# Kernel tuning notes

Hardware: AMD Instinct MI355X
Metric: run time of the kernel (lower is better)

Reference implementation:

```python
import jax, jax.numpy as jnp
import numpy as np

NUM_HEAD = 8
HEAD_SIZE = 32  # attention_size 256 / 8 heads


def setup_inputs() -> dict:
    key = jax.random.key(0)
    ks = jax.random.split(key, 10)
    B, S, H, A = 2, 4096, 256, 256
    x = jax.random.normal(ks[0], (B, S, H), dtype=jnp.float32)
    mask = jax.random.randint(ks[1], (B, S), 0, 2) > 0  # bool key-padding mask
    s = 0.02
    wq = jax.random.normal(ks[2], (A, H), dtype=jnp.float32) * s
    bq = jax.random.normal(ks[3], (A,), dtype=jnp.float32) * s
    wk = jax.random.normal(ks[4], (A, H), dtype=jnp.float32) * s
    bk = jax.random.normal(ks[5], (A,), dtype=jnp.float32) * s
    wv = jax.random.normal(ks[6], (A, H), dtype=jnp.float32) * s
    bv = jax.random.normal(ks[7], (A,), dtype=jnp.float32) * s
    wo = jax.random.normal(ks[8], (H, A), dtype=jnp.float32) * s
    bo = jax.random.normal(ks[9], (H,), dtype=jnp.float32) * s
    return {"x": x, "mask": mask, "wq": wq, "bq": bq, "wk": wk, "bk": bk,
            "wv": wv, "bv": bv, "wo": wo, "bo": bo}


def reference(x, mask, wq, bq, wk, bk, wv, bv, wo, bo):
    B, S, _ = x.shape
    # QKV projections -> [B, S, n_head, head_size]
    q = (x @ wq.T + bq).reshape(B, S, NUM_HEAD, HEAD_SIZE)
    k = (x @ wk.T + bk).reshape(B, S, NUM_HEAD, HEAD_SIZE)
    v = (x @ wv.T + bv).reshape(B, S, NUM_HEAD, HEAD_SIZE)
    # scores [B, H, Sq, Sk]
    attn = jnp.einsum('bqhd,bkhd->bhqk', q, k) / jnp.sqrt(
        jnp.asarray(HEAD_SIZE, dtype=x.dtype))
    # attn*mask - 1e5*~mask  ==  where(mask, attn, -1e5)
    attn = jnp.where(mask[:, None, None, :], attn, jnp.asarray(-100000.0, dtype=x.dtype))
    p = jax.nn.softmax(attn, axis=-1)
    o = jnp.einsum('bhqk,bkhd->bqhd', p, v).reshape(B, S, NUM_HEAD * HEAD_SIZE)
    return o @ wo.T + bo
```

## Files before the change

kernel.cpp:

```cpp
#include <hip/hip_runtime.h>

#define DEV __device__ __forceinline__

typedef __attribute__((ext_vector_type(8)))  short bf16x8;
typedef __attribute__((ext_vector_type(4)))  short s16x4;
typedef __attribute__((ext_vector_type(16))) float f32x16;

constexpr int SB = 2;
constexpr int SS = 4096;
constexpr int SH = 256;
constexpr int NHEAD = 8, HD = 32;
constexpr int M_TOK = SB * SS;
constexpr int NQKV = 3 * SH;

constexpr size_t OFF_CNT  = 0;
constexpr size_t OFF_BIAS = 256;
constexpr size_t OFF_XB   = OFF_BIAS + 32768;
constexpr size_t OFF_WQKV = OFF_XB + (size_t)M_TOK * SH * 2;
constexpr size_t OFF_BQKV = OFF_WQKV + (size_t)NQKV * SH * 2;
constexpr size_t OFF_WOB  = OFF_BQKV + 4096;
constexpr size_t OFF_BO   = OFF_WOB + (size_t)SH * SH * 2;
constexpr size_t OFF_Q    = OFF_BO + 1024;
constexpr size_t OFF_K    = OFF_Q + (size_t)M_TOK * SH * 2;
constexpr size_t OFF_V    = OFF_K + (size_t)M_TOK * SH * 2;
constexpr size_t OFF_VT   = OFF_V + (size_t)M_TOK * SH * 2;
constexpr size_t OFF_O    = OFF_VT + (size_t)M_TOK * SH * 2;
constexpr size_t WS_NEED  = OFF_O + (size_t)M_TOK * SH * 2;

DEV short f2bf(float f) {
  unsigned u = __builtin_bit_cast(unsigned, f);
  u = (u + 0x7FFFu + ((u >> 16) & 1u)) >> 16;
  return (short)u;
}

DEV float bf2f(short s) {
  return __builtin_bit_cast(float, ((unsigned)(unsigned short)s) << 16);
}

DEV float exp2_(float x) {
#if __has_builtin(__builtin_amdgcn_exp2f)
  return __builtin_amdgcn_exp2f(x);
#else
  float r;
  asm("v_exp_f32 %0, %1\n\ts_nop 0" : "=v"(r) : "v"(x));
  return r;
#endif
}

DEV unsigned cvtpk(float lo, float hi) {
  unsigned r;
  asm("v_cvt_pk_bf16_f32 %0, %1, %2" : "=v"(r) : "v"(lo), "v"(hi));
  return r;
}

DEV void plswap(unsigned& a, unsigned& b) {
  asm("v_permlane32_swap_b32 %0, %1" : "+v"(a), "+v"(b));
}

DEV float bperm_f(int srclane, float v) {
  int r = __builtin_amdgcn_ds_bpermute(srclane * 4, __builtin_bit_cast(int, v));
  return __builtin_bit_cast(float, r);
}

DEV void gll16(const short* g, short* l) {
  __builtin_amdgcn_global_load_lds(
      (const __attribute__((address_space(1))) void*)g,
      (__attribute__((address_space(3))) void*)l, 16, 0, 0);
}

__global__ void prep_kernel(const float* __restrict__ x,
    const float* __restrict__ wq, const float* __restrict__ bq,
    const float* __restrict__ wk, const float* __restrict__ bk,
    const float* __restrict__ wv, const float* __restrict__ bv,
    const float* __restrict__ wo, const float* __restrict__ bo,
    short* __restrict__ xb, short* __restrict__ Wqkv, float* __restrict__ bqkv,
    short* __restrict__ wob, float* __restrict__ bof) {
  const float QS = (float)(1.4426950408889634 / 5.656854249492381);
  long i = ((long)blockIdx.x * 256 + threadIdx.x) * 8;
  const long NX = (long)M_TOK * SH;
  const long NW = (long)NQKV * SH;
  if (i < NX) {
    const float4* s = (const float4*)(x + i);
    float4 f0 = s[0], f1 = s[1];
    bf16x8 o;
    o[0]=f2bf(f0.x); o[1]=f2bf(f0.y); o[2]=f2bf(f0.z); o[3]=f2bf(f0.w);
    o[4]=f2bf(f1.x); o[5]=f2bf(f1.y); o[6]=f2bf(f1.z); o[7]=f2bf(f1.w);
    *(bf16x8*)(xb + i) = o;
    return;
  }
  i -= NX;
  if (i < NW) {
    int n = (int)(i >> 8), kk = (int)(i & 255);
    int tn = n >> 8, rr = n & 255;
    const float* src = (tn == 0 ? wq : (tn == 1 ? wk : wv)) + rr * 256 + kk;
    float sc = tn == 0 ? QS : 1.f;
    float4 f0 = *(const float4*)src, f1 = *(const float4*)(src + 4);
    bf16x8 o;
    o[0]=f2bf(f0.x*sc); o[1]=f2bf(f0.y*sc); o[2]=f2bf(f0.z*sc); o[3]=f2bf(f0.w*sc);
    o[4]=f2bf(f1.x*sc); o[5]=f2bf(f1.y*sc); o[6]=f2bf(f1.z*sc); o[7]=f2bf(f1.w*sc);
    *(bf16x8*)(Wqkv + i) = o;
    return;
  }
  i -= NW;
  if (i < NQKV) {
    int n = (int)i;
#pragma unroll
    for (int j = 0; j < 8; ++j) {
      int nn = n + j, tn = nn >> 8, rr = nn & 255;
      const float* src = tn == 0 ? bq : (tn == 1 ? bk : bv);
      bqkv[nn] = src[rr] * (tn == 0 ? QS : 1.f);
    }
    return;
  }
  i -= NQKV;
  if (i < (long)SH * SH) {
    const float4* s = (const float4*)(wo + i);
    float4 f0 = s[0], f1 = s[1];
    bf16x8 o;
    o[0]=f2bf(f0.x); o[1]=f2bf(f0.y); o[2]=f2bf(f0.z); o[3]=f2bf(f0.w);
    o[4]=f2bf(f1.x); o[5]=f2bf(f1.y); o[6]=f2bf(f1.z); o[7]=f2bf(f1.w);
    *(bf16x8*)(wob + i) = o;
    return;
  }
  i -= (long)SH * SH;
  if (i < SH) {
#pragma unroll
    for (int j = 0; j < 8; ++j) bof[i + j] = bo[i + j];
  }
}

template <int MODE>
__global__ __launch_bounds__(256) void gemm_kernel(
    const short* __restrict__ Ag, const short* __restrict__ Bg,
    const float* __restrict__ bias,
    short* __restrict__ q, short* __restrict__ k, short* __restrict__ v,
    float* __restrict__ outf) {
  __shared__ __align__(16) short lA[8192];
  __shared__ __align__(16) short lB[4096];
  const int tid = threadIdx.x;
  const int lane = tid & 63, w = tid >> 6;
  const int wm = w >> 1, wn = w & 1;
  const int hi = lane >> 5, l31 = lane & 31;
  const int mb = blockIdx.x, nb = blockIdx.y;
  f32x16 acc0, acc1;
#pragma unroll
  for (int i = 0; i < 16; ++i) { acc0[i] = 0.f; acc1[i] = 0.f; }
  auto stage = [&](int kb) {
#pragma unroll
    for (int i = 0; i < 4; ++i) {
      int g = w * 256 + i * 64 + lane;
      int kg = g >> 7, m = g & 127;
      gll16(Ag + (size_t)(mb * 128 + m) * 256 + kb * 64 + kg * 8, lA + (size_t)g * 8);
    }
#pragma unroll
    for (int i = 0; i < 2; ++i) {
      int g = w * 128 + i * 64 + lane;
      int kg = g >> 6, n = g & 63;
      gll16(Bg + (size_t)(nb * 64 + n) * 256 + kb * 64 + kg * 8, lB + (size_t)g * 8);
    }
  };
  stage(0);
  for (int kb = 0; kb < 4; ++kb) {
    __syncthreads();
#pragma unroll
    for (int ks = 0; ks < 4; ++ks) {
      bf16x8 af0 = *(const bf16x8*)(lA + ((2 * ks + hi) * 128 + wm * 64 + l31) * 8);
      bf16x8 af1 = *(const bf16x8*)(lA + ((2 * ks + hi) * 128 + wm * 64 + 32 + l31) * 8);
      bf16x8 bf  = *(const bf16x8*)(lB + ((2 * ks + hi) * 64 + wn * 32 + l31) * 8);
      acc0 = __builtin_amdgcn_mfma_f32_32x32x16_bf16(af0, bf, acc0, 0, 0, 0);
      acc1 = __builtin_amdgcn_mfma_f32_32x32x16_bf16(af1, bf, acc1, 0, 0, 0);
    }
    __syncthreads();
    if (kb < 3) stage(kb + 1);
  }
  const int ncol = nb * 64 + wn * 32 + l31;
  const float bval = bias[ncol];
  if (MODE == 0) {
    const int tensor = nb >> 2;
    short* dst = tensor == 0 ? q : (tensor == 1 ? k : v);
    const int a = (nb & 3) * 64 + wn * 32 + l31;
    const int hh = a >> 5, d = a & 31;
#pragma unroll
    for (int mt = 0; mt < 2; ++mt) {
      const f32x16& acc = mt == 0 ? acc0 : acc1;
#pragma unroll
      for (int r = 0; r < 16; ++r) {
        int gm = mb * 128 + wm * 64 + mt * 32 + (r & 3) + 8 * (r >> 2) + 4 * hi;
        int bb = gm >> 12, ss = gm & 4095;
        dst[(((size_t)bb * NHEAD + hh) * SS + ss) * HD + d] = f2bf(acc[r] + bval);
      }
    }
  } else {
#pragma unroll
    for (int mt = 0; mt < 2; ++mt) {
      const f32x16& acc = mt == 0 ? acc0 : acc1;
#pragma unroll
      for (int r = 0; r < 16; ++r) {
        int gm = mb * 128 + wm * 64 + mt * 32 + (r & 3) + 8 * (r >> 2) + 4 * hi;
        outf[(size_t)gm * SH + ncol] = acc[r] + bval;
      }
    }
  }
}

__global__ void scan_mask_kernel(const unsigned char* __restrict__ m,
                                 int* __restrict__ idxC, int* __restrict__ cnts) {
  __shared__ int f_mis, f_off4, f_3f;
  __shared__ int ts[256];
  const int tid = threadIdx.x, b = blockIdx.x;
  if (tid == 0) { f_mis = 0; f_off4 = 0; f_3f = 0; }
  __syncthreads();
  int lm = 0, lo4 = 0, l3f = 0;
  for (int i = tid; i < 8192; i += 256) {
    unsigned char c = m[i];
    if (c) {
      if (i & 3) lm = 1;
      if ((i & 7) == 4) lo4 = 1;
      if ((i & 3) == 3 && c == 0x3F) l3f = 1;
    }
  }
  if (lm)  atomicOr(&f_mis, 1);
  if (lo4) atomicOr(&f_off4, 1);
  if (l3f) atomicOr(&f_3f, 1);
  __syncthreads();
  const int f = !f_mis ? (f_off4 ? 1 : 3) : (f_3f ? 2 : 0);
  int bits = 0;
  const int rbase = b * 4096 + tid * 16;
#pragma unroll
  for (int j = 0; j < 16; ++j) {
    int r = rbase + j;
    bool on;
    if (f == 0)      on = m[r] != 0;
    else if (f == 1) on = m[(size_t)r * 4] != 0;
    else if (f == 2) on = m[(size_t)r * 4 + 3] != 0;
    else             on = m[(size_t)r * 8] != 0;
    bits |= (int)on << j;
  }
  const int cnt = __popc(bits);
  ts[tid] = cnt;
  __syncthreads();
  for (int off = 1; off < 256; off <<= 1) {
    int u = (tid >= off) ? ts[tid - off] : 0;
    __syncthreads();
    ts[tid] += u;
    __syncthreads();
  }
  const int total = ts[255];
  int pos = ts[tid] - cnt;
  int* idxB = idxC + b * 4096;
  if (total == 0) {
    for (int j = tid; j < 4096; j += 256) idxB[j] = j;
    if (tid == 0) { cnts[b] = 4096; cnts[2 + b] = 4096; }
    return;
  }
#pragma unroll
  for (int j = 0; j < 16; ++j)
    if ((bits >> j) & 1) { idxB[pos] = tid * 16 + j; ++pos; }
  int cntpad = (total + 255) & ~255;
  if (cntpad < 256) cntpad = 256;
  for (int j = total + tid; j < cntpad; j += 256) idxB[j] = -1;
  if (tid == 0) { cnts[b] = cntpad; cnts[2 + b] = total; }
}

__global__ __launch_bounds__(256) void gather_kv_kernel(const short* __restrict__ K,
    const short* __restrict__ V, const int* __restrict__ idxC, const int* __restrict__ cnts,
    short* __restrict__ Kc, short* __restrict__ Vt) {
  const int bh = blockIdx.y, b = bh >> 3;
  const int jb = blockIdx.x * 64;
  if (jb >= cnts[b]) return;
  __shared__ short t[64][33];
  const int tid = threadIdx.x;
  const int s = tid >> 2, g = tid & 3;
  const int ix = idxC[b * 4096 + jb + s];
  bf16x8 kvv{}, vvv{};
  if (ix >= 0) {
    kvv = *(const bf16x8*)(K + ((size_t)bh * SS + ix) * HD + g * 8);
    vvv = *(const bf16x8*)(V + ((size_t)bh * SS + ix) * HD + g * 8);
  }
  *(bf16x8*)(Kc + ((size_t)bh * SS + jb + s) * HD + g * 8) = kvv;
#pragma unroll
  for (int j = 0; j < 8; ++j) t[s][g * 8 + j] = vvv[j];
  __syncthreads();
  const int d = tid >> 3, gs = tid & 7;
  bf16x8 out;
#pragma unroll
  for (int j = 0; j < 8; ++j) out[j] = t[gs * 8 + j][d];
  *(bf16x8*)(Vt + ((size_t)bh * HD + d) * SS + jb + gs * 8) = out;
}

__global__ __launch_bounds__(256, 2) void attn_kernel(const short* __restrict__ Q,
    const short* __restrict__ Kc, const short* __restrict__ Vt,
    const int* __restrict__ cnts,
    short* __restrict__ OP0, short* __restrict__ OP1, float* __restrict__ Lp) {
  __shared__ __align__(16) short sK[4096];
  __shared__ __align__(16) short sV[4096];
  const int tid = threadIdx.x;
  const int lane = tid & 63, wave = tid >> 6;
  const int hi = lane >> 5, l31 = lane & 31;
  const int qblk = blockIdx.x, bh = blockIdx.y, half = blockIdx.z;
  const int b = bh >> 3, h = bh & 7;
  const int Lh = cnts[b] >> 1;
  const int NIT = Lh >> 7;
  const int kv0 = half * Lh;
  const short* Kb = Kc + ((size_t)bh * SS + kv0) * HD;
  const short* Vb = Vt + (size_t)bh * HD * SS + kv0;
  const int qbase = qblk * 256 + wave * 64;
  const short* QrowA = Q + ((size_t)bh * SS + qbase + l31) * HD;
  const short* QrowB = QrowA + 32 * HD;
  const bf16x8 qa0 = *(const bf16x8*)(QrowA + hi * 8);
  const bf16x8 qa1 = *(const bf16x8*)(QrowA + 16 + hi * 8);
  const bf16x8 qb0 = *(const bf16x8*)(QrowB + hi * 8);
  const bf16x8 qb1 = *(const bf16x8*)(QrowB + 16 + hi * 8);
  f32x16 zro;
#pragma unroll
  for (int i = 0; i < 16; ++i) zro[i] = 0.f;
  f32x16 accA = zro, accB = zro;
  float lsA[4] = {0.f, 0.f, 0.f, 0.f};
  float lsB[4] = {0.f, 0.f, 0.f, 0.f};
  const int kgd = tid >> 6, kkv = tid & 63;
  const int vdv = tid & 31, vgk = tid >> 5;
  const short* kvsrc = Kb + (size_t)kkv * HD + kgd * 8;
  const short* vvsrc = Vb + (size_t)vdv * SS + vgk * 8;
  short* kdst0 = sK + ((size_t)kgd * 128 + kkv) * 8;
  short* kdst1 = kdst0 + 64 * 8;
  short* vdst0 = sV + ((size_t)vgk * 32 + vdv) * 8;
  short* vdst1 = vdst0 + 8 * 32 * 8;
  bf16x8 stgK0 = *(const bf16x8*)kvsrc;
  bf16x8 stgK1 = *(const bf16x8*)(kvsrc + 64 * HD);
  bf16x8 stgV0 = *(const bf16x8*)vvsrc;
  bf16x8 stgV1 = *(const bf16x8*)(vvsrc + 64);

  auto pack = [&](const f32x16& p, bf16x8& A, bf16x8& B) {
    unsigned a0 = cvtpk(p[0], p[1]),   a1 = cvtpk(p[2], p[3]);
    unsigned b0 = cvtpk(p[4], p[5]),   b1 = cvtpk(p[6], p[7]);
    plswap(a0, b0); plswap(a1, b1);
    unsigned c0 = cvtpk(p[8], p[9]),   c1 = cvtpk(p[10], p[11]);
    unsigned d0 = cvtpk(p[12], p[13]), d1 = cvtpk(p[14], p[15]);
    plswap(c0, d0); plswap(c1, d1);
    union { unsigned u[4]; bf16x8 v; } x, y;
    x.u[0] = a0; x.u[1] = a1; x.u[2] = b0; x.u[3] = b1;
    y.u[0] = c0; y.u[1] = c1; y.u[2] = d0; y.u[3] = d1;
    A = x.v; B = y.v;
  };

  for (int kt = 0; kt < NIT; ++kt) {
    __syncthreads();
    *(bf16x8*)kdst0 = stgK0;
    *(bf16x8*)kdst1 = stgK1;
    *(bf16x8*)vdst0 = stgV0;
    *(bf16x8*)vdst1 = stgV1;
    __syncthreads();
    if (kt + 1 < NIT) {
      const short* ks = kvsrc + (size_t)(kt + 1) * 128 * HD;
      stgK0 = *(const bf16x8*)ks;
      stgK1 = *(const bf16x8*)(ks + 64 * HD);
      const short* vs = vvsrc + (kt + 1) * 128;
      stgV0 = *(const bf16x8*)vs;
      stgV1 = *(const bf16x8*)(vs + 64);
    }
#pragma unroll
    for (int sub = 0; sub < 2; ++sub) {
      const int kb = sub * 64;
      const bf16x8 a00 = *(const bf16x8*)(sK + ((hi)*128 + kb + l31) * 8);
      const bf16x8 a01 = *(const bf16x8*)(sK + ((2 + hi) * 128 + kb + l31) * 8);
      const bf16x8 a10 = *(const bf16x8*)(sK + ((hi)*128 + kb + 32 + l31) * 8);
      const bf16x8 a11 = *(const bf16x8*)(sK + ((2 + hi) * 128 + kb + 32 + l31) * 8);
      const bf16x8 vb0 = *(const bf16x8*)(sV + ((sub * 8 + hi) * 32 + l31) * 8);
      const bf16x8 vb1 = *(const bf16x8*)(sV + ((sub * 8 + 2 + hi) * 32 + l31) * 8);
      const bf16x8 vb2 = *(const bf16x8*)(sV + ((sub * 8 + 4 + hi) * 32 + l31) * 8);
      const bf16x8 vb3 = *(const bf16x8*)(sV + ((sub * 8 + 6 + hi) * 32 + l31) * 8);
      f32x16 sA0 = __builtin_amdgcn_mfma_f32_32x32x16_bf16(a00, qa0, zro, 0, 0, 0);
      sA0 = __builtin_amdgcn_mfma_f32_32x32x16_bf16(a01, qa1, sA0, 0, 0, 0);
      f32x16 sA1 = __builtin_amdgcn_mfma_f32_32x32x16_bf16(a10, qa0, zro, 0, 0, 0);
      sA1 = __builtin_amdgcn_mfma_f32_32x32x16_bf16(a11, qa1, sA1, 0, 0, 0);
      f32x16 sB0 = __builtin_amdgcn_mfma_f32_32x32x16_bf16(a00, qb0, zro, 0, 0, 0);
      sB0 = __builtin_amdgcn_mfma_f32_32x32x16_bf16(a01, qb1, sB0, 0, 0, 0);
      f32x16 sB1 = __builtin_amdgcn_mfma_f32_32x32x16_bf16(a10, qb0, zro, 0, 0, 0);
      sB1 = __builtin_amdgcn_mfma_f32_32x32x16_bf16(a11, qb1, sB1, 0, 0, 0);
      f32x16 p;
#pragma unroll
      for (int r = 0; r < 16; ++r) { p[r] = exp2_(sA0[r]); lsA[r & 3] += p[r]; }
      bf16x8 pa1, pa2;
      pack(p, pa1, pa2);
#pragma unroll
      for (int r = 0; r < 16; ++r) { p[r] = exp2_(sA1[r]); lsA[r & 3] += p[r]; }
      bf16x8 pa3, pa4;
      pack(p, pa3, pa4);
      accA = __builtin_amdgcn_mfma_f32_32x32x16_bf16(pa1, vb0, accA, 0, 0, 0);
      accA = __builtin_amdgcn_mfma_f32_32x32x16_bf16(pa2, vb1, accA, 0, 0, 0);
      accA = __builtin_amdgcn_mfma_f32_32x32x16_bf16(pa3, vb2, accA, 0, 0, 0);
      accA = __builtin_amdgcn_mfma_f32_32x32x16_bf16(pa4, vb3, accA, 0, 0, 0);
#pragma unroll
      for (int r = 0; r < 16; ++r) { p[r] = exp2_(sB0[r]); lsB[r & 3] += p[r]; }
      bf16x8 pb1, pb2;
      pack(p, pb1, pb2);
#pragma unroll
      for (int r = 0; r < 16; ++r) { p[r] = exp2_(sB1[r]); lsB[r & 3] += p[r]; }
      bf16x8 pb3, pb4;
      pack(p, pb3, pb4);
      accB = __builtin_amdgcn_mfma_f32_32x32x16_bf16(pb1, vb0, accB, 0, 0, 0);
      accB = __builtin_amdgcn_mfma_f32_32x32x16_bf16(pb2, vb1, accB, 0, 0, 0);
      accB = __builtin_amdgcn_mfma_f32_32x32x16_bf16(pb3, vb2, accB, 0, 0, 0);
      accB = __builtin_amdgcn_mfma_f32_32x32x16_bf16(pb4, vb3, accB, 0, 0, 0);
    }
  }
  float fsA = (lsA[0] + lsA[1]) + (lsA[2] + lsA[3]);
  float fsB = (lsB[0] + lsB[1]) + (lsB[2] + lsB[3]);
  fsA += __shfl_xor(fsA, 32);
  fsB += __shfl_xor(fsB, 32);
  short* OP = half ? OP1 : OP0;
#pragma unroll
  for (int r = 0; r < 16; ++r) {
    int qq = (r & 3) + 8 * (r >> 2) + 4 * hi;
    int mA = b * SS + qbase + qq;
    OP[(size_t)mA * SH + h * HD + l31] = f2bf(accA[r]);
    int mB = mA + 32;
    OP[(size_t)mB * SH + h * HD + l31] = f2bf(accB[r]);
    float lvA = bperm_f(qq, fsA);
    float lvB = bperm_f(qq, fsB);
    if (l31 == 0) {
      Lp[((size_t)half * 16 + bh) * SS + qbase + qq] = lvA;
      Lp[((size_t)half * 16 + bh) * SS + qbase + 32 + qq] = lvB;
    }
  }
}

__global__ __launch_bounds__(256) void combine_kernel(const short* __restrict__ P0,
    const short* __restrict__ P1, const float* __restrict__ Lp,
    const int* __restrict__ cnts, short* __restrict__ Ow) {
  int t = blockIdx.x * 256 + threadIdx.x;
  int m = t >> 6, c4 = (t & 63) * 4;
  int b = m >> 12, s = m & 4095, h = c4 >> 5;
  s16x4 o0 = *(const s16x4*)(P0 + (size_t)m * SH + c4);
  s16x4 o1 = *(const s16x4*)(P1 + (size_t)m * SH + c4);
  int bh = b * 8 + h;
  float npad = (float)(cnts[b] - cnts[2 + b]);
  float l = Lp[(size_t)bh * SS + s] + Lp[((size_t)16 + bh) * SS + s] - npad;
  float rcp = 1.f / l;
  s16x4 out;
#pragma unroll
  for (int j = 0; j < 4; ++j) out[j] = f2bf((bf2f(o0[j]) + bf2f(o1[j])) * rcp);
  *(s16x4*)(Ow + (size_t)m * SH + c4) = out;
}

extern "C" void kernel_launch(void* const* d_in, const int* in_sizes, int n_in,
                              void* d_out, int out_size, void* d_ws, size_t ws_size,
                              hipStream_t stream) {
  (void)in_sizes; (void)n_in; (void)out_size;
  if (ws_size < WS_NEED) return;
  const float* x  = (const float*)d_in[0];
  const unsigned char* mask = (const unsigned char*)d_in[1];
  const float* wq = (const float*)d_in[2];
  const float* bq = (const float*)d_in[3];
  const float* wk = (const float*)d_in[4];
  const float* bk = (const float*)d_in[5];
  const float* wv = (const float*)d_in[6];
  const float* bv = (const float*)d_in[7];
  const float* wo = (const float*)d_in[8];
  const float* bo = (const float*)d_in[9];
  char* ws = (char*)d_ws;
  int*   cnts    = (int*)(ws + OFF_CNT);
  short* xb      = (short*)(ws + OFF_XB);
  short* Wqkv    = (short*)(ws + OFF_WQKV);
  float* bqkv    = (float*)(ws + OFF_BQKV);
  short* wob     = (short*)(ws + OFF_WOB);
  float* bof     = (float*)(ws + OFF_BO);
  short* Qw      = (short*)(ws + OFF_Q);
  short* Kw      = (short*)(ws + OFF_K);
  short* Vw      = (short*)(ws + OFF_V);
  short* Vtw     = (short*)(ws + OFF_VT);
  short* Kc      = (short*)(ws + OFF_XB);
  int*   idxC    = (int*)(ws + OFF_WQKV);
  short* OP0     = (short*)(ws + OFF_K);
  short* OP1     = (short*)(ws + OFF_V);
  float* Lp      = (float*)(ws + OFF_O);

  prep_kernel<<<1153, 256, 0, stream>>>(x, wq, bq, wk, bk, wv, bv, wo, bo,
                                        xb, Wqkv, bqkv, wob, bof);
  gemm_kernel<0><<<dim3(64, 12), 256, 0, stream>>>(xb, Wqkv, bqkv, Qw, Kw, Vw, nullptr);
  scan_mask_kernel<<<2, 256, 0, stream>>>(mask, idxC, cnts);
  gather_kv_kernel<<<dim3(64, 16), 256, 0, stream>>>(Kw, Vw, idxC, cnts, Kc, Vtw);
  attn_kernel<<<dim3(16, 16, 2), 256, 0, stream>>>(Qw, Kc, Vtw, cnts, OP0, OP1, Lp);
  combine_kernel<<<2048, 256, 0, stream>>>(OP0, OP1, Lp, cnts, OP0);
  gemm_kernel<1><<<dim3(64, 4), 256, 0, stream>>>(OP0, wob, bof,
                                                  nullptr, nullptr, nullptr, (float*)d_out);
}
```

Measured before the change: 85.73 us.

## Stage GEMM tiles through registers and prefetch next k-block during MFMA

Replaces the direct global-to-LDS loads in the projection GEMM with ordinary vector loads into registers, followed by an explicit store to LDS. The next k-block's global loads are now issued before the MFMA loop on the current tile, so memory latency can overlap with compute instead of stalling after each block. It also changes the global access pattern so each thread reads 8 consecutive bf16 along K for a row, which should give coalesced 128-byte row segments. The cost is extra VGPRs for the staging registers and explicit LDS write instructions.

```diff
diff --git a/kernel.cpp b/kernel.cpp
--- a/kernel.cpp
+++ b/kernel.cpp
@@ -60,12 +60,6 @@
 DEV float bperm_f(int srclane, float v) {
   int r = __builtin_amdgcn_ds_bpermute(srclane * 4, __builtin_bit_cast(int, v));
   return __builtin_bit_cast(float, r);
-}
-
-DEV void gll16(const short* g, short* l) {
-  __builtin_amdgcn_global_load_lds(
-      (const __attribute__((address_space(1))) void*)g,
-      (__attribute__((address_space(3))) void*)l, 16, 0, 0);
 }
 
 __global__ void prep_kernel(const float* __restrict__ x,
@@ -145,23 +139,27 @@
   f32x16 acc0, acc1;
 #pragma unroll
   for (int i = 0; i < 16; ++i) { acc0[i] = 0.f; acc1[i] = 0.f; }
-  auto stage = [&](int kb) {
-#pragma unroll
-    for (int i = 0; i < 4; ++i) {
-      int g = w * 256 + i * 64 + lane;
-      int kg = g >> 7, m = g & 127;
-      gll16(Ag + (size_t)(mb * 128 + m) * 256 + kb * 64 + kg * 8, lA + (size_t)g * 8);
-    }
-#pragma unroll
-    for (int i = 0; i < 2; ++i) {
-      int g = w * 128 + i * 64 + lane;
-      int kg = g >> 6, n = g & 63;
-      gll16(Bg + (size_t)(nb * 64 + n) * 256 + kb * 64 + kg * 8, lB + (size_t)g * 8);
-    }
+  bf16x8 ra[4], rb[2];
+  const int am = tid >> 3, ak = tid & 7;
+  auto gload = [&](int kb) {
+#pragma unroll
+    for (int p = 0; p < 4; ++p)
+      ra[p] = *(const bf16x8*)(Ag + (size_t)(mb * 128 + p * 32 + am) * 256 + kb * 64 + ak * 8);
+#pragma unroll
+    for (int p = 0; p < 2; ++p)
+      rb[p] = *(const bf16x8*)(Bg + (size_t)(nb * 64 + p * 32 + am) * 256 + kb * 64 + ak * 8);
   };
-  stage(0);
+  gload(0);
   for (int kb = 0; kb < 4; ++kb) {
     __syncthreads();
+#pragma unroll
+    for (int p = 0; p < 4; ++p)
+      *(bf16x8*)(lA + (ak * 128 + p * 32 + am) * 8) = ra[p];
+#pragma unroll
+    for (int p = 0; p < 2; ++p)
+      *(bf16x8*)(lB + (ak * 64 + p * 32 + am) * 8) = rb[p];
+    __syncthreads();
+    if (kb < 3) gload(kb + 1);
 #pragma unroll
     for (int ks = 0; ks < 4; ++ks) {
       bf16x8 af0 = *(const bf16x8*)(lA + ((2 * ks + hi) * 128 + wm * 64 + l31) * 8);
@@ -170,8 +168,6 @@
       acc0 = __builtin_amdgcn_mfma_f32_32x32x16_bf16(af0, bf, acc0, 0, 0, 0);
       acc1 = __builtin_amdgcn_mfma_f32_32x32x16_bf16(af1, bf, acc1, 0, 0, 0);
     }
-    __syncthreads();
-    if (kb < 3) stage(kb + 1);
   }
   const int ncol = nb * 64 + wn * 32 + l31;
   const float bval = bias[ncol];
```

After: 84.59 us. No clear change (-1.3%).
